# Kernel tuning notes

Hardware: AMD Instinct MI355X
Metric: run time of the kernel (lower is better)

The kernel has to match this reference:

```python
import jax, jax.numpy as jnp
import numpy as np

N = 100000   # nodes
E = 1200000  # edges
B = 128      # graphs per batch
F = 92       # raw node features
D = 64       # pre_hidden_size == gc_dim == post_hidden_size
L = 3        # n_gcn
Z = 2 * D + 1  # CGConv concat width


def setup_inputs() -> dict:
    key = jax.random.key(0)
    ks = jax.random.split(key, 24)
    s = 0.1
    inp = {
        "X": jax.random.normal(ks[0], (N, F), jnp.float32),
        "edge_idx": jax.random.randint(ks[1], (2, E), 0, N),
        "edge_weight": jax.random.uniform(ks[2], (E,), jnp.float32),
        "edge_attr": jax.random.normal(ks[3], (E,), jnp.float32),
        "batch_map": jnp.sort(jax.random.randint(ks[4], (N,), 0, B)),
        # pre-GCN MLP: F->D, D->D, D->D, relu after each
        "pre_W0": jax.random.normal(ks[5], (F, D)) * s,
        "pre_b0": jnp.zeros((D,), jnp.float32),
        "pre_W1": jax.random.normal(ks[6], (D, D)) * s,
        "pre_b1": jnp.zeros((D,), jnp.float32),
        "pre_W2": jax.random.normal(ks[7], (D, D)) * s,
        "pre_b2": jnp.zeros((D,), jnp.float32),
        # CGConv gates: lin_f / lin_s: (2D+1)->D, stacked over L layers
        "cg_Wf": jax.random.normal(ks[8], (L, Z, D)) * s,
        "cg_bf": jnp.zeros((L, D), jnp.float32),
        "cg_Ws": jax.random.normal(ks[9], (L, Z, D)) * s,
        "cg_bs": jnp.zeros((L, D), jnp.float32),
        # post-GCN MLP: D->D x3 (relu) then D->1
        "post_W0": jax.random.normal(ks[10], (D, D)) * s,
        "post_b0": jnp.zeros((D,), jnp.float32),
        "post_W1": jax.random.normal(ks[11], (D, D)) * s,
        "post_b1": jnp.zeros((D,), jnp.float32),
        "post_W2": jax.random.normal(ks[12], (D, D)) * s,
        "post_b2": jnp.zeros((D,), jnp.float32),
        "post_Wf": jax.random.normal(ks[13], (D, 1)) * s,
        "post_bf": jnp.zeros((1,), jnp.float32),
    }
    return inp


def _forward(X, edge_idx, edge_weight, edge_attr, batch_map,
             pre_W0, pre_b0, pre_W1, pre_b1, pre_W2, pre_b2,
             cg_Wf, cg_bf, cg_Ws, cg_bs,
             post_W0, post_b0, post_W1, post_b1, post_W2, post_b2,
             post_Wf, post_bf):
    relu = jax.nn.relu
    # pre-GC MLP
    h = relu(X @ pre_W0 + pre_b0)
    h = relu(h @ pre_W1 + pre_b1)
    h = relu(h @ pre_W2 + pre_b2)  # [N, D]

    src = edge_idx[0]  # x_j (message source)
    dst = edge_idx[1]  # x_i (aggregation target)
    ea = edge_attr.reshape(-1, 1)  # [E, 1]
    # in-degree for mean aggregation (nodes with no edges -> 0 via denom clamp)
    deg = jax.ops.segment_sum(jnp.ones((E,), h.dtype), dst, num_segments=N)
    denom = jnp.maximum(deg, 1.0)[:, None]  # [N, 1]

    for l in range(L):
        # CGConv: z = [x_i || x_j || e], out = x + mean_i(sigmoid(z Wf) * softplus(z Ws))
        z = jnp.concatenate([h[dst], h[src], ea], axis=-1)  # [E, 2D+1]
        m = jax.nn.sigmoid(z @ cg_Wf[l] + cg_bf[l]) * jax.nn.softplus(z @ cg_Ws[l] + cg_bs[l])
        agg = jax.ops.segment_sum(m, dst, num_segments=N) / denom
        h = relu(h + agg)  # residual + activation from pyg Sequential

    # early global mean pool per graph
    gsum = jax.ops.segment_sum(h, batch_map, num_segments=B)
    gcnt = jax.ops.segment_sum(jnp.ones((N,), h.dtype), batch_map, num_segments=B)
    g = gsum / jnp.maximum(gcnt, 1.0)[:, None]  # [B, D]

    # post-GC MLP
    g = relu(g @ post_W0 + post_b0)
    g = relu(g @ post_W1 + post_b1)
    g = relu(g @ post_W2 + post_b2)
    return g @ post_Wf + post_bf  # [B, 1]


def reference(X, edge_idx, edge_weight, edge_attr, batch_map,
              pre_W0, pre_b0, pre_W1, pre_b1, pre_W2, pre_b2,
              cg_Wf, cg_bf, cg_Ws, cg_bs,
              post_W0, post_b0, post_W1, post_b1, post_W2, post_b2,
              post_Wf, post_bf):
    return _forward(X, edge_idx, edge_weight, edge_attr, batch_map,
                    pre_W0, pre_b0, pre_W1, pre_b1, pre_W2, pre_b2,
                    cg_Wf, cg_bf, cg_Ws, cg_bs,
                    post_W0, post_b0, post_W1, post_b1, post_W2, post_b2,
                    post_Wf, post_bf)
```

## Files before the change

kernel.cpp:

```cpp
#include <hip/hip_runtime.h>
#include <hip/hip_bf16.h>
#include <math.h>

#define GN 100000
#define GE 1200000
#define GB 128
#define GF 92
#define GD 64
#define GL 3
#define GZ 129

#define HS 65

__device__ __forceinline__ unsigned int f2bf_rne(float x)
{
    unsigned int u = __float_as_uint(x);
    u += 0x7fffu + ((u >> 16) & 1u);
    return u >> 16;
}

__global__ __launch_bounds__(256, 2) void premlp_kernel(
    const float* __restrict__ X,
    const float* __restrict__ W0, const float* __restrict__ b0,
    const float* __restrict__ W1, const float* __restrict__ b1,
    const float* __restrict__ W2, const float* __restrict__ b2,
    const float* __restrict__ WfD, const float* __restrict__ WsD,
    const float* __restrict__ WfS, const float* __restrict__ WsS,
    const float* __restrict__ bf, const float* __restrict__ bs,
    float* __restrict__ hout, unsigned int* __restrict__ Pout,
    float* __restrict__ Qout, int N)
{
    __shared__ __align__(16) float Wl[5888];
    __shared__ float hl[128 * HS];
    const int tid = threadIdx.x;
    const int lane = tid & 63;
    const int col0 = (tid >> 6) * 16;
    const int base = blockIdx.x * 128;
    const int n0 = base + lane;
    const int n1 = base + 64 + lane;
    const int nn0 = (n0 < N) ? n0 : (N - 1);
    const int nn1 = (n1 < N) ? n1 : (N - 1);
    const bool act0 = (n0 < N), act1 = (n1 < N);

    float a0[16], a1[16], s0[16], s1[16];

    {
        const float4* __restrict__ s4 = (const float4*)W0;
        float4* __restrict__ d4 = (float4*)Wl;
        for (int i = tid; i < 1472; i += 256) d4[i] = s4[i];
    }
    __syncthreads();

#pragma unroll
    for (int j = 0; j < 16; ++j) { a0[j] = b0[col0 + j]; a1[j] = a0[j]; }
    {
        const float4* __restrict__ r40 = (const float4*)(X + (size_t)nn0 * GF);
        const float4* __restrict__ r41 = (const float4*)(X + (size_t)nn1 * GF);
        for (int c = 0; c < 23; ++c) {
            float4 v0 = r40[c];
            float4 v1 = r41[c];
            const float* __restrict__ w = Wl + c * 256 + col0;
#pragma unroll
            for (int j = 0; j < 16; ++j) {
                float wa = w[j], wb = w[64 + j], wc = w[128 + j], wd = w[192 + j];
                a0[j] = fmaf(v0.x, wa, a0[j]);
                a0[j] = fmaf(v0.y, wb, a0[j]);
                a0[j] = fmaf(v0.z, wc, a0[j]);
                a0[j] = fmaf(v0.w, wd, a0[j]);
                a1[j] = fmaf(v1.x, wa, a1[j]);
                a1[j] = fmaf(v1.y, wb, a1[j]);
                a1[j] = fmaf(v1.z, wc, a1[j]);
                a1[j] = fmaf(v1.w, wd, a1[j]);
            }
        }
    }
    __syncthreads();
#pragma unroll
    for (int j = 0; j < 16; ++j) {
        hl[lane * HS + col0 + j] = fmaxf(a0[j], 0.f);
        hl[(64 + lane) * HS + col0 + j] = fmaxf(a1[j], 0.f);
    }
    {
        const float4* __restrict__ s4 = (const float4*)W1;
        float4* __restrict__ d4 = (float4*)Wl;
        for (int i = tid; i < 1024; i += 256) d4[i] = s4[i];
    }
    __syncthreads();

#pragma unroll
    for (int j = 0; j < 16; ++j) { a0[j] = b1[col0 + j]; a1[j] = a0[j]; }
    for (int c = 0; c < 16; ++c) {
        float h0 = hl[lane * HS + 4 * c + 0];
        float h1 = hl[lane * HS + 4 * c + 1];
        float h2 = hl[lane * HS + 4 * c + 2];
        float h3 = hl[lane * HS + 4 * c + 3];
        float g0 = hl[(64 + lane) * HS + 4 * c + 0];
        float g1 = hl[(64 + lane) * HS + 4 * c + 1];
        float g2 = hl[(64 + lane) * HS + 4 * c + 2];
        float g3 = hl[(64 + lane) * HS + 4 * c + 3];
        const float* __restrict__ w = Wl + c * 256 + col0;
#pragma unroll
        for (int j = 0; j < 16; ++j) {
            float wa = w[j], wb = w[64 + j], wc = w[128 + j], wd = w[192 + j];
            a0[j] = fmaf(h0, wa, a0[j]);
            a0[j] = fmaf(h1, wb, a0[j]);
            a0[j] = fmaf(h2, wc, a0[j]);
            a0[j] = fmaf(h3, wd, a0[j]);
            a1[j] = fmaf(g0, wa, a1[j]);
            a1[j] = fmaf(g1, wb, a1[j]);
            a1[j] = fmaf(g2, wc, a1[j]);
            a1[j] = fmaf(g3, wd, a1[j]);
        }
    }
    __syncthreads();
#pragma unroll
    for (int j = 0; j < 16; ++j) {
        hl[lane * HS + col0 + j] = fmaxf(a0[j], 0.f);
        hl[(64 + lane) * HS + col0 + j] = fmaxf(a1[j], 0.f);
    }
    {
        const float4* __restrict__ s4 = (const float4*)W2;
        float4* __restrict__ d4 = (float4*)Wl;
        for (int i = tid; i < 1024; i += 256) d4[i] = s4[i];
    }
    __syncthreads();

#pragma unroll
    for (int j = 0; j < 16; ++j) { a0[j] = b2[col0 + j]; a1[j] = a0[j]; }
    for (int c = 0; c < 16; ++c) {
        float h0 = hl[lane * HS + 4 * c + 0];
        float h1 = hl[lane * HS + 4 * c + 1];
        float h2 = hl[lane * HS + 4 * c + 2];
        float h3 = hl[lane * HS + 4 * c + 3];
        float g0 = hl[(64 + lane) * HS + 4 * c + 0];
        float g1 = hl[(64 + lane) * HS + 4 * c + 1];
        float g2 = hl[(64 + lane) * HS + 4 * c + 2];
        float g3 = hl[(64 + lane) * HS + 4 * c + 3];
        const float* __restrict__ w = Wl + c * 256 + col0;
#pragma unroll
        for (int j = 0; j < 16; ++j) {
            float wa = w[j], wb = w[64 + j], wc = w[128 + j], wd = w[192 + j];
            a0[j] = fmaf(h0, wa, a0[j]);
            a0[j] = fmaf(h1, wb, a0[j]);
            a0[j] = fmaf(h2, wc, a0[j]);
            a0[j] = fmaf(h3, wd, a0[j]);
            a1[j] = fmaf(g0, wa, a1[j]);
            a1[j] = fmaf(g1, wb, a1[j]);
            a1[j] = fmaf(g2, wc, a1[j]);
            a1[j] = fmaf(g3, wd, a1[j]);
        }
    }
    __syncthreads();
#pragma unroll
    for (int j = 0; j < 16; ++j) {
        hl[lane * HS + col0 + j] = fmaxf(a0[j], 0.f);
        hl[(64 + lane) * HS + col0 + j] = fmaxf(a1[j], 0.f);
    }
    if (act0) {
        float4* __restrict__ op = (float4*)(hout + (size_t)n0 * 64 + col0);
#pragma unroll
        for (int q = 0; q < 4; ++q)
            op[q] = make_float4(fmaxf(a0[q * 4], 0.f), fmaxf(a0[q * 4 + 1], 0.f),
                                fmaxf(a0[q * 4 + 2], 0.f), fmaxf(a0[q * 4 + 3], 0.f));
    }
    if (act1) {
        float4* __restrict__ op = (float4*)(hout + (size_t)n1 * 64 + col0);
#pragma unroll
        for (int q = 0; q < 4; ++q)
            op[q] = make_float4(fmaxf(a1[q * 4], 0.f), fmaxf(a1[q * 4 + 1], 0.f),
                                fmaxf(a1[q * 4 + 2], 0.f), fmaxf(a1[q * 4 + 3], 0.f));
    }
    {
        const float4* __restrict__ s4 = (const float4*)WfS;
        float4* __restrict__ d4 = (float4*)Wl;
        for (int i = tid; i < 1024; i += 256) d4[i] = s4[i];
    }
    __syncthreads();

#pragma unroll
    for (int j = 0; j < 16; ++j) { a0[j] = 0.f; a1[j] = 0.f; }
    for (int c = 0; c < 16; ++c) {
        float h0 = hl[lane * HS + 4 * c + 0];
        float h1 = hl[lane * HS + 4 * c + 1];
        float h2 = hl[lane * HS + 4 * c + 2];
        float h3 = hl[lane * HS + 4 * c + 3];
        float g0 = hl[(64 + lane) * HS + 4 * c + 0];
        float g1 = hl[(64 + lane) * HS + 4 * c + 1];
        float g2 = hl[(64 + lane) * HS + 4 * c + 2];
        float g3 = hl[(64 + lane) * HS + 4 * c + 3];
        const float* __restrict__ w = Wl + c * 256 + col0;
#pragma unroll
        for (int j = 0; j < 16; ++j) {
            float wa = w[j], wb = w[64 + j], wc = w[128 + j], wd = w[192 + j];
            a0[j] = fmaf(h0, wa, a0[j]);
            a0[j] = fmaf(h1, wb, a0[j]);
            a0[j] = fmaf(h2, wc, a0[j]);
            a0[j] = fmaf(h3, wd, a0[j]);
            a1[j] = fmaf(g0, wa, a1[j]);
            a1[j] = fmaf(g1, wb, a1[j]);
            a1[j] = fmaf(g2, wc, a1[j]);
            a1[j] = fmaf(g3, wd, a1[j]);
        }
    }
    __syncthreads();
    {
        const float4* __restrict__ s4 = (const float4*)WsS;
        float4* __restrict__ d4 = (float4*)Wl;
        for (int i = tid; i < 1024; i += 256) d4[i] = s4[i];
    }
    __syncthreads();

#pragma unroll
    for (int j = 0; j < 16; ++j) { s0[j] = 0.f; s1[j] = 0.f; }
    for (int c = 0; c < 16; ++c) {
        float h0 = hl[lane * HS + 4 * c + 0];
        float h1 = hl[lane * HS + 4 * c + 1];
        float h2 = hl[lane * HS + 4 * c + 2];
        float h3 = hl[lane * HS + 4 * c + 3];
        float g0 = hl[(64 + lane) * HS + 4 * c + 0];
        float g1 = hl[(64 + lane) * HS + 4 * c + 1];
        float g2 = hl[(64 + lane) * HS + 4 * c + 2];
        float g3 = hl[(64 + lane) * HS + 4 * c + 3];
        const float* __restrict__ w = Wl + c * 256 + col0;
#pragma unroll
        for (int j = 0; j < 16; ++j) {
            float wa = w[j], wb = w[64 + j], wc = w[128 + j], wd = w[192 + j];
            s0[j] = fmaf(h0, wa, s0[j]);
            s0[j] = fmaf(h1, wb, s0[j]);
            s0[j] = fmaf(h2, wc, s0[j]);
            s0[j] = fmaf(h3, wd, s0[j]);
            s1[j] = fmaf(g0, wa, s1[j]);
            s1[j] = fmaf(g1, wb, s1[j]);
            s1[j] = fmaf(g2, wc, s1[j]);
            s1[j] = fmaf(g3, wd, s1[j]);
        }
    }
    if (act0) {
        uint4* __restrict__ pp = (uint4*)(Pout + (size_t)n0 * 64 + col0);
#pragma unroll
        for (int q = 0; q < 4; ++q) {
            uint4 pk;
            pk.x = f2bf_rne(a0[q * 4])     | (f2bf_rne(s0[q * 4]) << 16);
            pk.y = f2bf_rne(a0[q * 4 + 1]) | (f2bf_rne(s0[q * 4 + 1]) << 16);
            pk.z = f2bf_rne(a0[q * 4 + 2]) | (f2bf_rne(s0[q * 4 + 2]) << 16);
            pk.w = f2bf_rne(a0[q * 4 + 3]) | (f2bf_rne(s0[q * 4 + 3]) << 16);
            pp[q] = pk;
        }
    }
    if (act1) {
        uint4* __restrict__ pp = (uint4*)(Pout + (size_t)n1 * 64 + col0);
#pragma unroll
        for (int q = 0; q < 4; ++q) {
            uint4 pk;
            pk.x = f2bf_rne(a1[q * 4])     | (f2bf_rne(s1[q * 4]) << 16);
            pk.y = f2bf_rne(a1[q * 4 + 1]) | (f2bf_rne(s1[q * 4 + 1]) << 16);
            pk.z = f2bf_rne(a1[q * 4 + 2]) | (f2bf_rne(s1[q * 4 + 2]) << 16);
            pk.w = f2bf_rne(a1[q * 4 + 3]) | (f2bf_rne(s1[q * 4 + 3]) << 16);
            pp[q] = pk;
        }
    }
    __syncthreads();
    {
        const float4* __restrict__ s4 = (const float4*)WfD;
        float4* __restrict__ d4 = (float4*)Wl;
        for (int i = tid; i < 1024; i += 256) d4[i] = s4[i];
    }
    __syncthreads();

#pragma unroll
    for (int j = 0; j < 16; ++j) { a0[j] = bf[col0 + j]; a1[j] = a0[j]; }
    for (int c = 0; c < 16; ++c) {
        float h0 = hl[lane * HS + 4 * c + 0];
        float h1 = hl[lane * HS + 4 * c + 1];
        float h2 = hl[lane * HS + 4 * c + 2];
        float h3 = hl[lane * HS + 4 * c + 3];
        float g0 = hl[(64 + lane) * HS + 4 * c + 0];
        float g1 = hl[(64 + lane) * HS + 4 * c + 1];
        float g2 = hl[(64 + lane) * HS + 4 * c + 2];
        float g3 = hl[(64 + lane) * HS + 4 * c + 3];
        const float* __restrict__ w = Wl + c * 256 + col0;
#pragma unroll
        for (int j = 0; j < 16; ++j) {
            float wa = w[j], wb = w[64 + j], wc = w[128 + j], wd = w[192 + j];
            a0[j] = fmaf(h0, wa, a0[j]);
            a0[j] = fmaf(h1, wb, a0[j]);
            a0[j] = fmaf(h2, wc, a0[j]);
            a0[j] = fmaf(h3, wd, a0[j]);
            a1[j] = fmaf(g0, wa, a1[j]);
            a1[j] = fmaf(g1, wb, a1[j]);
            a1[j] = fmaf(g2, wc, a1[j]);
            a1[j] = fmaf(g3, wd, a1[j]);
        }
    }
    __syncthreads();
    {
        const float4* __restrict__ s4 = (const float4*)WsD;
        float4* __restrict__ d4 = (float4*)Wl;
        for (int i = tid; i < 1024; i += 256) d4[i] = s4[i];
    }
    __syncthreads();

#pragma unroll
    for (int j = 0; j < 16; ++j) { s0[j] = bs[col0 + j]; s1[j] = s0[j]; }
    for (int c = 0; c < 16; ++c) {
        float h0 = hl[lane * HS + 4 * c + 0];
        float h1 = hl[lane * HS + 4 * c + 1];
        float h2 = hl[lane * HS + 4 * c + 2];
        float h3 = hl[lane * HS + 4 * c + 3];
        float g0 = hl[(64 + lane) * HS + 4 * c + 0];
        float g1 = hl[(64 + lane) * HS + 4 * c + 1];
        float g2 = hl[(64 + lane) * HS + 4 * c + 2];
        float g3 = hl[(64 + lane) * HS + 4 * c + 3];
        const float* __restrict__ w = Wl + c * 256 + col0;
#pragma unroll
        for (int j = 0; j < 16; ++j) {
            float wa = w[j], wb = w[64 + j], wc = w[128 + j], wd = w[192 + j];
            s0[j] = fmaf(h0, wa, s0[j]);
            s0[j] = fmaf(h1, wb, s0[j]);
            s0[j] = fmaf(h2, wc, s0[j]);
            s0[j] = fmaf(h3, wd, s0[j]);
            s1[j] = fmaf(g0, wa, s1[j]);
            s1[j] = fmaf(g1, wb, s1[j]);
            s1[j] = fmaf(g2, wc, s1[j]);
            s1[j] = fmaf(g3, wd, s1[j]);
        }
    }
    if (act0) {
        float4* __restrict__ qp = (float4*)(Qout + (size_t)n0 * 128 + col0 * 2);
#pragma unroll
        for (int q = 0; q < 8; ++q)
            qp[q] = make_float4(a0[q * 2], s0[q * 2], a0[q * 2 + 1], s0[q * 2 + 1]);
    }
    if (act1) {
        float4* __restrict__ qp = (float4*)(Qout + (size_t)n1 * 128 + col0 * 2);
#pragma unroll
        for (int q = 0; q < 8; ++q)
            qp[q] = make_float4(a1[q * 2], s1[q * 2], a1[q * 2 + 1], s1[q * 2 + 1]);
    }
}

__global__ __launch_bounds__(256, 3) void pjq_kernel(
    const float* __restrict__ h,
    const float* __restrict__ Wf, const float* __restrict__ Ws,
    const float* __restrict__ bfv, const float* __restrict__ bsv,
    unsigned int* __restrict__ P, float* __restrict__ Q, int N)
{
    __shared__ __align__(16) float Wl[4096];
    __shared__ float hl[128 * HS];
    const int tid = threadIdx.x;
    const int lane = tid & 63;
    const int col0 = (tid >> 6) * 16;
    const int base = blockIdx.x * 128;
    const int n0 = base + lane;
    const int n1 = base + 64 + lane;
    const bool act0 = (n0 < N), act1 = (n1 < N);

    float a0[16], a1[16], s0[16], s1[16];

    for (int q = tid; q < 2048; q += 256) {
        int r = q >> 4, c4 = q & 15;
        int rr = base + r; rr = (rr < N) ? rr : (N - 1);
        float4 v = ((const float4*)(h + (size_t)rr * 64))[c4];
        float* dp = hl + r * HS + c4 * 4;
        dp[0] = v.x; dp[1] = v.y; dp[2] = v.z; dp[3] = v.w;
    }
    {
        const float4* __restrict__ s4 = (const float4*)(Wf + 64 * 64);
        float4* __restrict__ d4 = (float4*)Wl;
        for (int i = tid; i < 1024; i += 256) d4[i] = s4[i];
    }
    __syncthreads();

#pragma unroll
    for (int j = 0; j < 16; ++j) { a0[j] = 0.f; a1[j] = 0.f; }
    for (int c = 0; c < 16; ++c) {
        float h0 = hl[lane * HS + 4 * c + 0];
        float h1 = hl[lane * HS + 4 * c + 1];
        float h2 = hl[lane * HS + 4 * c + 2];
        float h3 = hl[lane * HS + 4 * c + 3];
        float g0 = hl[(64 + lane) * HS + 4 * c + 0];
        float g1 = hl[(64 + lane) * HS + 4 * c + 1];
        float g2 = hl[(64 + lane) * HS + 4 * c + 2];
        float g3 = hl[(64 + lane) * HS + 4 * c + 3];
        const float* __restrict__ w = Wl + c * 256 + col0;
#pragma unroll
        for (int j = 0; j < 16; ++j) {
            float wa = w[j], wb = w[64 + j], wc = w[128 + j], wd = w[192 + j];
            a0[j] = fmaf(h0, wa, a0[j]);
            a0[j] = fmaf(h1, wb, a0[j]);
            a0[j] = fmaf(h2, wc, a0[j]);
            a0[j] = fmaf(h3, wd, a0[j]);
            a1[j] = fmaf(g0, wa, a1[j]);
            a1[j] = fmaf(g1, wb, a1[j]);
            a1[j] = fmaf(g2, wc, a1[j]);
            a1[j] = fmaf(g3, wd, a1[j]);
        }
    }
    __syncthreads();
    {
        const float4* __restrict__ s4 = (const float4*)(Ws + 64 * 64);
        float4* __restrict__ d4 = (float4*)Wl;
        for (int i = tid; i < 1024; i += 256) d4[i] = s4[i];
    }
    __syncthreads();

#pragma unroll
    for (int j = 0; j < 16; ++j) { s0[j] = 0.f; s1[j] = 0.f; }
    for (int c = 0; c < 16; ++c) {
        float h0 = hl[lane * HS + 4 * c + 0];
        float h1 = hl[lane * HS + 4 * c + 1];
        float h2 = hl[lane * HS + 4 * c + 2];
        float h3 = hl[lane * HS + 4 * c + 3];
        float g0 = hl[(64 + lane) * HS + 4 * c + 0];
        float g1 = hl[(64 + lane) * HS + 4 * c + 1];
        float g2 = hl[(64 + lane) * HS + 4 * c + 2];
        float g3 = hl[(64 + lane) * HS + 4 * c + 3];
        const float* __restrict__ w = Wl + c * 256 + col0;
#pragma unroll
        for (int j = 0; j < 16; ++j) {
            float wa = w[j], wb = w[64 + j], wc = w[128 + j], wd = w[192 + j];
            s0[j] = fmaf(h0, wa, s0[j]);
            s0[j] = fmaf(h1, wb, s0[j]);
            s0[j] = fmaf(h2, wc, s0[j]);
            s0[j] = fmaf(h3, wd, s0[j]);
            s1[j] = fmaf(g0, wa, s1[j]);
            s1[j] = fmaf(g1, wb, s1[j]);
            s1[j] = fmaf(g2, wc, s1[j]);
            s1[j] = fmaf(g3, wd, s1[j]);
        }
    }
    if (act0) {
        uint4* __restrict__ pp = (uint4*)(P + (size_t)n0 * 64 + col0);
#pragma unroll
        for (int q = 0; q < 4; ++q) {
            uint4 pk;
            pk.x = f2bf_rne(a0[q * 4])     | (f2bf_rne(s0[q * 4]) << 16);
            pk.y = f2bf_rne(a0[q * 4 + 1]) | (f2bf_rne(s0[q * 4 + 1]) << 16);
            pk.z = f2bf_rne(a0[q * 4 + 2]) | (f2bf_rne(s0[q * 4 + 2]) << 16);
            pk.w = f2bf_rne(a0[q * 4 + 3]) | (f2bf_rne(s0[q * 4 + 3]) << 16);
            pp[q] = pk;
        }
    }
    if (act1) {
        uint4* __restrict__ pp = (uint4*)(P + (size_t)n1 * 64 + col0);
#pragma unroll
        for (int q = 0; q < 4; ++q) {
            uint4 pk;
            pk.x = f2bf_rne(a1[q * 4])     | (f2bf_rne(s1[q * 4]) << 16);
            pk.y = f2bf_rne(a1[q * 4 + 1]) | (f2bf_rne(s1[q * 4 + 1]) << 16);
            pk.z = f2bf_rne(a1[q * 4 + 2]) | (f2bf_rne(s1[q * 4 + 2]) << 16);
            pk.w = f2bf_rne(a1[q * 4 + 3]) | (f2bf_rne(s1[q * 4 + 3]) << 16);
            pp[q] = pk;
        }
    }
    __syncthreads();
    {
        const float4* __restrict__ s4 = (const float4*)Wf;
        float4* __restrict__ d4 = (float4*)Wl;
        for (int i = tid; i < 1024; i += 256) d4[i] = s4[i];
    }
    __syncthreads();

#pragma unroll
    for (int j = 0; j < 16; ++j) { a0[j] = bfv[col0 + j]; a1[j] = a0[j]; }
    for (int c = 0; c < 16; ++c) {
        float h0 = hl[lane * HS + 4 * c + 0];
        float h1 = hl[lane * HS + 4 * c + 1];
        float h2 = hl[lane * HS + 4 * c + 2];
        float h3 = hl[lane * HS + 4 * c + 3];
        float g0 = hl[(64 + lane) * HS + 4 * c + 0];
        float g1 = hl[(64 + lane) * HS + 4 * c + 1];
        float g2 = hl[(64 + lane) * HS + 4 * c + 2];
        float g3 = hl[(64 + lane) * HS + 4 * c + 3];
        const float* __restrict__ w = Wl + c * 256 + col0;
#pragma unroll
        for (int j = 0; j < 16; ++j) {
            float wa = w[j], wb = w[64 + j], wc = w[128 + j], wd = w[192 + j];
            a0[j] = fmaf(h0, wa, a0[j]);
            a0[j] = fmaf(h1, wb, a0[j]);
            a0[j] = fmaf(h2, wc, a0[j]);
            a0[j] = fmaf(h3, wd, a0[j]);
            a1[j] = fmaf(g0, wa, a1[j]);
            a1[j] = fmaf(g1, wb, a1[j]);
            a1[j] = fmaf(g2, wc, a1[j]);
            a1[j] = fmaf(g3, wd, a1[j]);
        }
    }
    __syncthreads();
    {
        const float4* __restrict__ s4 = (const float4*)Ws;
        float4* __restrict__ d4 = (float4*)Wl;
        for (int i = tid; i < 1024; i += 256) d4[i] = s4[i];
    }
    __syncthreads();

#pragma unroll
    for (int j = 0; j < 16; ++j) { s0[j] = bsv[col0 + j]; s1[j] = s0[j]; }
    for (int c = 0; c < 16; ++c) {
        float h0 = hl[lane * HS + 4 * c + 0];
        float h1 = hl[lane * HS + 4 * c + 1];
        float h2 = hl[lane * HS + 4 * c + 2];
        float h3 = hl[lane * HS + 4 * c + 3];
        float g0 = hl[(64 + lane) * HS + 4 * c + 0];
        float g1 = hl[(64 + lane) * HS + 4 * c + 1];
        float g2 = hl[(64 + lane) * HS + 4 * c + 2];
        float g3 = hl[(64 + lane) * HS + 4 * c + 3];
        const float* __restrict__ w = Wl + c * 256 + col0;
#pragma unroll
        for (int j = 0; j < 16; ++j) {
            float wa = w[j], wb = w[64 + j], wc = w[128 + j], wd = w[192 + j];
            s0[j] = fmaf(h0, wa, s0[j]);
            s0[j] = fmaf(h1, wb, s0[j]);
            s0[j] = fmaf(h2, wc, s0[j]);
            s0[j] = fmaf(h3, wd, s0[j]);
            s1[j] = fmaf(g0, wa, s1[j]);
            s1[j] = fmaf(g1, wb, s1[j]);
            s1[j] = fmaf(g2, wc, s1[j]);
            s1[j] = fmaf(g3, wd, s1[j]);
        }
    }
    if (act0) {
        float4* __restrict__ qp = (float4*)(Q + (size_t)n0 * 128 + col0 * 2);
#pragma unroll
        for (int q = 0; q < 8; ++q)
            qp[q] = make_float4(a0[q * 2], s0[q * 2], a0[q * 2 + 1], s0[q * 2 + 1]);
    }
    if (act1) {
        float4* __restrict__ qp = (float4*)(Q + (size_t)n1 * 128 + col0 * 2);
#pragma unroll
        for (int q = 0; q < 8; ++q)
            qp[q] = make_float4(a1[q * 2], s1[q * 2], a1[q * 2 + 1], s1[q * 2 + 1]);
    }
}

__global__ __launch_bounds__(256) void deg_kernel(
    const int* __restrict__ dst, int* __restrict__ deg, int E)
{
    int e = blockIdx.x * blockDim.x + threadIdx.x;
    if (e < E) atomicAdd(&deg[dst[e]], 1);
}

__global__ __launch_bounds__(1024) void scanA_kernel(
    const int* __restrict__ deg, int* __restrict__ iscan,
    int* __restrict__ bsum, int N)
{
    __shared__ int lds[1024];
    int tid = threadIdx.x;
    int gid = blockIdx.x * 1024 + tid;
    int v = (gid < N) ? deg[gid] : 0;
    lds[tid] = v; __syncthreads();
    for (int off = 1; off < 1024; off <<= 1) {
        int t = (tid >= off) ? lds[tid - off] : 0;
        __syncthreads();
        lds[tid] += t;
        __syncthreads();
    }
    if (gid < N) iscan[gid] = lds[tid];
    if (tid == 1023) bsum[blockIdx.x] = lds[1023];
}

__global__ __launch_bounds__(128) void scanB_kernel(
    const int* __restrict__ bsum, int* __restrict__ boff, int nb)
{
    __shared__ int lds[128];
    int t = threadIdx.x;
    int v = (t < nb) ? bsum[t] : 0;
    lds[t] = v; __syncthreads();
    for (int off = 1; off < 128; off <<= 1) {
        int u = (t >= off) ? lds[t - off] : 0;
        __syncthreads();
        lds[t] += u;
        __syncthreads();
    }
    if (t < nb) boff[t] = lds[t] - v;
}

__global__ __launch_bounds__(256) void scanC_kernel(
    const int* __restrict__ iscan, const int* __restrict__ boff,
    const int* __restrict__ deg,
    int* __restrict__ rowptr, int* __restrict__ cursor, int N)
{
    int i = blockIdx.x * blockDim.x + threadIdx.x;
    if (i >= N) return;
    int incl = iscan[i] + boff[i >> 10];
    rowptr[i + 1] = incl;
    cursor[i] = incl - deg[i];
    if (i == 0) rowptr[0] = 0;
}

__global__ __launch_bounds__(256) void escatter_kernel(
    const int* __restrict__ src, const int* __restrict__ dst,
    const float* __restrict__ ea, int* __restrict__ cursor,
    int2* __restrict__ e_se, int E)
{
    int e = blockIdx.x * blockDim.x + threadIdx.x;
    if (e >= E) return;
    int pos = atomicAdd(&cursor[dst[e]], 1);
    e_se[pos] = make_int2(src[e], __float_as_int(ea[e]));
}

__global__ __launch_bounds__(256) void edge_kernel(
    const float* __restrict__ h, const int* __restrict__ rowptr,
    const int2* __restrict__ e_se,
    const unsigned int* __restrict__ P,
    const float* __restrict__ Q,
    const float* __restrict__ Wf, const float* __restrict__ Ws,
    float* __restrict__ hout)
{
    int n = blockIdx.x * 4 + (threadIdx.x >> 6);
    int d = threadIdx.x & 63;

    const float2 qv = ((const float2*)Q)[(size_t)n * 64 + d];
    float qf = qv.x, qs = qv.y;
    float wf = Wf[128 * 64 + d];
    float ws = Ws[128 * 64 + d];

    size_t idx = (size_t)n * 64 + d;
    float hres = h[idx];

    int rb = rowptr[n], re = rowptr[n + 1];
    float agg = 0.f;
#pragma unroll 8
    for (int p = rb; p < re; ++p) {
        int2 se = e_se[p];
        int s = se.x;
        float ea = __int_as_float(se.y);
        unsigned int pv = P[(size_t)s * 64 + d];
        float pf = __uint_as_float(pv << 16);
        float psv = __uint_as_float(pv & 0xffff0000u);
        float xF = fmaf(ea, wf, qf + pf);
        float xS = fmaf(ea, ws, qs + psv);
        float sig = __builtin_amdgcn_rcpf(1.f + __expf(-xF));
        float t = __expf(-fabsf(xS));
        float sp = fmaxf(xS, 0.f) + __logf(1.f + t);
        agg = fmaf(sig, sp, agg);
    }

    float inv = 1.f / (float)max(re - rb, 1);
    hout[idx] = fmaxf(hres + agg * inv, 0.f);
}

__global__ __launch_bounds__(256) void gstart_kernel(
    const int* __restrict__ bm, int* __restrict__ gstart, int N)
{
    int i = blockIdx.x * blockDim.x + threadIdx.x;
    if (i >= N) return;
    int b = bm[i];
    int prev = (i == 0) ? -1 : bm[i - 1];
    for (int g = prev + 1; g <= b; ++g) gstart[g] = i;
    if (i == N - 1)
        for (int g = b + 1; g <= GB; ++g) gstart[g] = N;
}

__global__ __launch_bounds__(256) void pool_seg_kernel(
    const float* __restrict__ h, const int* __restrict__ gstart,
    float* __restrict__ g)
{
    int b = blockIdx.x;
    int s = gstart[b], e = gstart[b + 1];
    int d = threadIdx.x & 63;
    int w = threadIdx.x >> 6;
    float acc = 0.f;
    for (int n = s + w; n < e; n += 4)
        acc += h[(size_t)n * 64 + d];
    __shared__ float lds[256];
    lds[threadIdx.x] = acc;
    __syncthreads();
    if (w == 0) {
        acc = lds[d] + lds[64 + d] + lds[128 + d] + lds[192 + d];
        g[b * 64 + d] = acc / fmaxf((float)(e - s), 1.f);
    }
}

__global__ __launch_bounds__(256) void postmlp_kernel(
    const float* __restrict__ g,
    const float* __restrict__ W0, const float* __restrict__ b0,
    const float* __restrict__ W1, const float* __restrict__ b1,
    const float* __restrict__ W2, const float* __restrict__ b2,
    const float* __restrict__ Wfin, const float* __restrict__ bfin,
    float* __restrict__ out)
{
    int b = blockIdx.x * 4 + (threadIdx.x >> 6);
    int d = threadIdx.x & 63;
    float h = g[(size_t)b * 64 + d];

    float acc = b0[d];
#pragma unroll
    for (int k = 0; k < 64; ++k)
        acc = fmaf(__shfl(h, k, 64), W0[k * 64 + d], acc);
    h = fmaxf(acc, 0.f);

    acc = b1[d];
#pragma unroll
    for (int k = 0; k < 64; ++k)
        acc = fmaf(__shfl(h, k, 64), W1[k * 64 + d], acc);
    h = fmaxf(acc, 0.f);

    acc = b2[d];
#pragma unroll
    for (int k = 0; k < 64; ++k)
        acc = fmaf(__shfl(h, k, 64), W2[k * 64 + d], acc);
    h = fmaxf(acc, 0.f);

    float v = h * Wfin[d];
#pragma unroll
    for (int off = 32; off >= 1; off >>= 1)
        v += __shfl_xor(v, off, 64);
    if (d == 0) out[b] = v + bfin[0];
}

extern "C" void kernel_launch(void* const* d_in, const int* in_sizes, int n_in,
                              void* d_out, int out_size, void* d_ws, size_t ws_size,
                              hipStream_t stream)
{
    const float* X      = (const float*)d_in[0];
    const int*   eidx   = (const int*)d_in[1];
    const float* ea     = (const float*)d_in[3];
    const int*   bm     = (const int*)d_in[4];
    const float* pre_W0 = (const float*)d_in[5];
    const float* pre_b0 = (const float*)d_in[6];
    const float* pre_W1 = (const float*)d_in[7];
    const float* pre_b1 = (const float*)d_in[8];
    const float* pre_W2 = (const float*)d_in[9];
    const float* pre_b2 = (const float*)d_in[10];
    const float* cg_Wf  = (const float*)d_in[11];
    const float* cg_bf  = (const float*)d_in[12];
    const float* cg_Ws  = (const float*)d_in[13];
    const float* cg_bs  = (const float*)d_in[14];
    const float* post_W0 = (const float*)d_in[15];
    const float* post_b0 = (const float*)d_in[16];
    const float* post_W1 = (const float*)d_in[17];
    const float* post_b1 = (const float*)d_in[18];
    const float* post_W2 = (const float*)d_in[19];
    const float* post_b2 = (const float*)d_in[20];
    const float* post_Wf = (const float*)d_in[21];
    const float* post_bf = (const float*)d_in[22];

    const int* src = eidx;
    const int* dst = eidx + GE;

    const size_t N64 = (size_t)GN * 64;
    float* hA    = (float*)d_ws;
    float* hB    = hA + N64;
    unsigned int* P = (unsigned int*)(hB + N64);
    int* deg_i   = (int*)(P + N64);
    int* iscan   = deg_i + GN;
    int* bsum    = iscan + GN;
    int* boff    = bsum + 128;
    int* rowptr  = boff + 128;
    int* cursor  = rowptr + GN + 2;
    int2* e_se   = (int2*)(cursor + GN);
    int* gstart  = (int*)(e_se + GE);
    float* g0    = (float*)(gstart + GB + 1);
    float* Q     = g0 + (size_t)GB * 64;

    const int TPB = 256;
    int gridE  = (GE + TPB - 1) / TPB;
    int gridN  = (GN + TPB - 1) / TPB;
    int gridP  = (GN + 127) / 128;
    int gridND = ((GN * 64) + TPB - 1) / TPB;
    int scanBlocks = (GN + 1023) / 1024;

    const float* Wf0 = cg_Wf;
    const float* Ws0 = cg_Ws;
    const float* Wf1 = cg_Wf + (size_t)1 * GZ * GD;
    const float* Ws1 = cg_Ws + (size_t)1 * GZ * GD;
    const float* Wf2 = cg_Wf + (size_t)2 * GZ * GD;
    const float* Ws2 = cg_Ws + (size_t)2 * GZ * GD;

    premlp_kernel<<<gridP, TPB, 0, stream>>>(
        X, pre_W0, pre_b0, pre_W1, pre_b1, pre_W2, pre_b2,
        Wf0, Ws0, Wf0 + 64 * 64, Ws0 + 64 * 64, cg_bf, cg_bs,
        hA, P, Q, GN);

    hipMemsetAsync(deg_i, 0, GN * sizeof(int), stream);
    deg_kernel<<<gridE, TPB, 0, stream>>>(dst, deg_i, GE);
    scanA_kernel<<<scanBlocks, 1024, 0, stream>>>(deg_i, iscan, bsum, GN);
    scanB_kernel<<<1, 128, 0, stream>>>(bsum, boff, scanBlocks);
    scanC_kernel<<<gridN, TPB, 0, stream>>>(iscan, boff, deg_i, rowptr, cursor, GN);
    escatter_kernel<<<gridE, TPB, 0, stream>>>(src, dst, ea, cursor, e_se, GE);

    gstart_kernel<<<gridN, TPB, 0, stream>>>(bm, gstart, GN);

    edge_kernel<<<gridND, TPB, 0, stream>>>(
        hA, rowptr, e_se, P, Q, Wf0, Ws0, hB);
    pjq_kernel<<<gridP, TPB, 0, stream>>>(
        hB, Wf1, Ws1, cg_bf + GD, cg_bs + GD, P, Q, GN);
    edge_kernel<<<gridND, TPB, 0, stream>>>(
        hB, rowptr, e_se, P, Q, Wf1, Ws1, hA);
    pjq_kernel<<<gridP, TPB, 0, stream>>>(
        hA, Wf2, Ws2, cg_bf + 2 * GD, cg_bs + 2 * GD, P, Q, GN);
    edge_kernel<<<gridND, TPB, 0, stream>>>(
        hA, rowptr, e_se, P, Q, Wf2, Ws2, hB);

    pool_seg_kernel<<<GB, TPB, 0, stream>>>(hB, gstart, g0);

    postmlp_kernel<<<GB / 4, TPB, 0, stream>>>(
        g0, post_W0, post_b0, post_W1, post_b1, post_W2, post_b2,
        post_Wf, post_bf, (float*)d_out);
}
```

Baseline: 884.0 us.

## Switch CGConv aggregation to edge-parallel chunks with atomic segment flushes

Replaces the node-per-wavefront edge loop with an edge-parallel kernel. Each wavefront processes a fixed chunk of 32 dst-sorted edges and flushes partial sums via atomicAdd when the destination changes. A separate finalize kernel applies the mean, residual and ReLU, then re-zeroes the accumulator. This targets load imbalance from the variable in-degree, at the cost of float atomics, a wider 16-byte edge record, an extra N×64 buffer and one extra kernel launch per layer.

```diff
diff --git a/kernel.cpp b/kernel.cpp
--- a/kernel.cpp
+++ b/kernel.cpp
@@ -11,6 +11,7 @@
 #define GZ 129
 
 #define HS 65
+#define EC 32
 
 __device__ __forceinline__ unsigned int f2bf_rne(float x)
 {
@@ -591,41 +592,44 @@
 __global__ __launch_bounds__(256) void escatter_kernel(
     const int* __restrict__ src, const int* __restrict__ dst,
     const float* __restrict__ ea, int* __restrict__ cursor,
-    int2* __restrict__ e_se, int E)
+    int4* __restrict__ e_sd, int E)
 {
     int e = blockIdx.x * blockDim.x + threadIdx.x;
     if (e >= E) return;
-    int pos = atomicAdd(&cursor[dst[e]], 1);
-    e_se[pos] = make_int2(src[e], __float_as_int(ea[e]));
-}
-
-__global__ __launch_bounds__(256) void edge_kernel(
-    const float* __restrict__ h, const int* __restrict__ rowptr,
-    const int2* __restrict__ e_se,
+    int d = dst[e];
+    int pos = atomicAdd(&cursor[d], 1);
+    e_sd[pos] = make_int4(src[e], __float_as_int(ea[e]), d, 0);
+}
+
+__global__ __launch_bounds__(256) void edgepar_kernel(
+    const int4* __restrict__ e_sd,
     const unsigned int* __restrict__ P,
     const float* __restrict__ Q,
     const float* __restrict__ Wf, const float* __restrict__ Ws,
-    float* __restrict__ hout)
-{
-    int n = blockIdx.x * 4 + (threadIdx.x >> 6);
-    int d = threadIdx.x & 63;
-
-    const float2 qv = ((const float2*)Q)[(size_t)n * 64 + d];
-    float qf = qv.x, qs = qv.y;
-    float wf = Wf[128 * 64 + d];
-    float ws = Ws[128 * 64 + d];
-
-    size_t idx = (size_t)n * 64 + d;
-    float hres = h[idx];
-
-    int rb = rowptr[n], re = rowptr[n + 1];
-    float agg = 0.f;
-#pragma unroll 8
-    for (int p = rb; p < re; ++p) {
-        int2 se = e_se[p];
-        int s = se.x;
+    float* __restrict__ agg, int E)
+{
+    const int lane = threadIdx.x & 63;
+    const int wid = blockIdx.x * 4 + (threadIdx.x >> 6);
+    int c0 = wid * EC;
+    if (c0 >= E) return;
+    int ce = min(c0 + EC, E);
+
+    const float wf = Wf[128 * 64 + lane];
+    const float ws = Ws[128 * 64 + lane];
+
+    int cur = -1;
+    float acc = 0.f, qf = 0.f, qs = 0.f;
+    for (int c = c0; c < ce; ++c) {
+        int4 se = e_sd[c];
+        unsigned int pv = P[(size_t)se.x * 64 + lane];
+        if (se.z != cur) {
+            if (cur >= 0) atomicAdd(&agg[(size_t)cur * 64 + lane], acc);
+            acc = 0.f;
+            cur = se.z;
+            float2 qv = ((const float2*)Q)[(size_t)cur * 64 + lane];
+            qf = qv.x; qs = qv.y;
+        }
         float ea = __int_as_float(se.y);
-        unsigned int pv = P[(size_t)s * 64 + d];
         float pf = __uint_as_float(pv << 16);
         float psv = __uint_as_float(pv & 0xffff0000u);
         float xF = fmaf(ea, wf, qf + pf);
@@ -633,11 +637,22 @@
         float sig = __builtin_amdgcn_rcpf(1.f + __expf(-xF));
         float t = __expf(-fabsf(xS));
         float sp = fmaxf(xS, 0.f) + __logf(1.f + t);
-        agg = fmaf(sig, sp, agg);
-    }
-
-    float inv = 1.f / (float)max(re - rb, 1);
-    hout[idx] = fmaxf(hres + agg * inv, 0.f);
+        acc = fmaf(sig, sp, acc);
+    }
+    atomicAdd(&agg[(size_t)cur * 64 + lane], acc);
+}
+
+__global__ __launch_bounds__(256) void finalize_kernel(
+    const float* __restrict__ hin, const int* __restrict__ deg,
+    float* __restrict__ agg, float* __restrict__ hout, int total)
+{
+    int i = blockIdx.x * 256 + threadIdx.x;
+    if (i >= total) return;
+    int n = i >> 6;
+    float a = agg[i];
+    agg[i] = 0.f;
+    float inv = 1.f / (float)max(deg[n], 1);
+    hout[i] = fmaxf(hin[i] + a * inv, 0.f);
 }
 
 __global__ __launch_bounds__(256) void gstart_kernel(
@@ -743,22 +758,24 @@
     float* hA    = (float*)d_ws;
     float* hB    = hA + N64;
     unsigned int* P = (unsigned int*)(hB + N64);
-    int* deg_i   = (int*)(P + N64);
+    float* agg   = (float*)(P + N64);
+    float* Q     = agg + N64;
+    int4* e_sd   = (int4*)(Q + (size_t)GN * 128);
+    int* deg_i   = (int*)(e_sd + GE);
     int* iscan   = deg_i + GN;
     int* bsum    = iscan + GN;
     int* boff    = bsum + 128;
     int* rowptr  = boff + 128;
     int* cursor  = rowptr + GN + 2;
-    int2* e_se   = (int2*)(cursor + GN);
-    int* gstart  = (int*)(e_se + GE);
+    int* gstart  = cursor + GN;
     float* g0    = (float*)(gstart + GB + 1);
-    float* Q     = g0 + (size_t)GB * 64;
 
     const int TPB = 256;
     int gridE  = (GE + TPB - 1) / TPB;
     int gridN  = (GN + TPB - 1) / TPB;
     int gridP  = (GN + 127) / 128;
     int gridND = ((GN * 64) + TPB - 1) / TPB;
+    int gridEP = (GE + EC * 4 - 1) / (EC * 4);
     int scanBlocks = (GN + 1023) / 1024;
 
     const float* Wf0 = cg_Wf;
@@ -774,24 +791,27 @@
         hA, P, Q, GN);
 
     hipMemsetAsync(deg_i, 0, GN * sizeof(int), stream);
+    hipMemsetAsync(agg, 0, N64 * sizeof(float), stream);
     deg_kernel<<<gridE, TPB, 0, stream>>>(dst, deg_i, GE);
     scanA_kernel<<<scanBlocks, 1024, 0, stream>>>(deg_i, iscan, bsum, GN);
     scanB_kernel<<<1, 128, 0, stream>>>(bsum, boff, scanBlocks);
     scanC_kernel<<<gridN, TPB, 0, stream>>>(iscan, boff, deg_i, rowptr, cursor, GN);
-    escatter_kernel<<<gridE, TPB, 0, stream>>>(src, dst, ea, cursor, e_se, GE);
+    escatter_kernel<<<gridE, TPB, 0, stream>>>(src, dst, ea, cursor, e_sd, GE);
 
     gstart_kernel<<<gridN, TPB, 0, stream>>>(bm, gstart, GN);
 
-    edge_kernel<<<gridND, TPB, 0, stream>>>(
-        hA, rowptr, e_se, P, Q, Wf0, Ws0, hB);
+    edgepar_kernel<<<gridEP, TPB, 0, stream>>>(e_sd, P, Q, Wf0, Ws0, agg, GE);
+    finalize_kernel<<<gridND, TPB, 0, stream>>>(hA, deg_i, agg, hB, GN * 64);
     pjq_kernel<<<gridP, TPB, 0, stream>>>(
         hB, Wf1, Ws1, cg_bf + GD, cg_bs + GD, P, Q, GN);
-    edge_kernel<<<gridND, TPB, 0, stream>>>(
-        hB, rowptr, e_se, P, Q, Wf1, Ws1, hA);
+
+    edgepar_kernel<<<gridEP, TPB, 0, stream>>>(e_sd, P, Q, Wf1, Ws1, agg, GE);
+    finalize_kernel<<<gridND, TPB, 0, stream>>>(hB, deg_i, agg, hA, GN * 64);
     pjq_kernel<<<gridP, TPB, 0, stream>>>(
         hA, Wf2, Ws2, cg_bf + 2 * GD, cg_bs + 2 * GD, P, Q, GN);
-    edge_kernel<<<gridND, TPB, 0, stream>>>(
-        hA, rowptr, e_se, P, Q, Wf2, Ws2, hB);
+
+    edgepar_kernel<<<gridEP, TPB, 0, stream>>>(e_sd, P, Q, Wf2, Ws2, agg, GE);
+    finalize_kernel<<<gridND, TPB, 0, stream>>>(hA, deg_i, agg, hB, GN * 64);
 
     pool_seg_kernel<<<GB, TPB, 0, stream>>>(hB, gstart, g0);
 
```

After: 1.038 ms. +17.4%, slower.

## Fuse f/s gate GEMMs in pjq kernel and read h rows directly from global

Applied to the files above, without the earlier changes.

The pjq kernel now stages the Wf and Ws tiles together in a doubled shared buffer and computes both gate projections in one pass, instead of four sequential weight loads separated by barriers. It also drops the shared-memory staging of h: each thread reads its node's row straight from global memory as float4, so all four wavefronts in a block reload the same rows. This removes several barriers and the h LDS traffic. In exchange, register pressure rises (64 live accumulators under launch_bounds 256,3) and global h reads are repeated across wavefronts and across the two passes.

```diff
diff --git a/kernel.cpp b/kernel.cpp
--- a/kernel.cpp
+++ b/kernel.cpp
@@ -345,88 +345,60 @@
     const float* __restrict__ bfv, const float* __restrict__ bsv,
     unsigned int* __restrict__ P, float* __restrict__ Q, int N)
 {
-    __shared__ __align__(16) float Wl[4096];
-    __shared__ float hl[128 * HS];
+    __shared__ __align__(16) float Wl[8192];
     const int tid = threadIdx.x;
     const int lane = tid & 63;
     const int col0 = (tid >> 6) * 16;
     const int base = blockIdx.x * 128;
     const int n0 = base + lane;
     const int n1 = base + 64 + lane;
+    const int nn0 = (n0 < N) ? n0 : (N - 1);
+    const int nn1 = (n1 < N) ? n1 : (N - 1);
     const bool act0 = (n0 < N), act1 = (n1 < N);
 
-    float a0[16], a1[16], s0[16], s1[16];
-
-    for (int q = tid; q < 2048; q += 256) {
-        int r = q >> 4, c4 = q & 15;
-        int rr = base + r; rr = (rr < N) ? rr : (N - 1);
-        float4 v = ((const float4*)(h + (size_t)rr * 64))[c4];
-        float* dp = hl + r * HS + c4 * 4;
-        dp[0] = v.x; dp[1] = v.y; dp[2] = v.z; dp[3] = v.w;
-    }
-    {
-        const float4* __restrict__ s4 = (const float4*)(Wf + 64 * 64);
-        float4* __restrict__ d4 = (float4*)Wl;
-        for (int i = tid; i < 1024; i += 256) d4[i] = s4[i];
-    }
-    __syncthreads();
-
-#pragma unroll
-    for (int j = 0; j < 16; ++j) { a0[j] = 0.f; a1[j] = 0.f; }
+    const float4* __restrict__ h40 = (const float4*)(h + (size_t)nn0 * 64);
+    const float4* __restrict__ h41 = (const float4*)(h + (size_t)nn1 * 64);
+
+    float aF0[16], aF1[16], aS0[16], aS1[16];
+
+    {
+        const float4* __restrict__ f4 = (const float4*)(Wf + 64 * 64);
+        const float4* __restrict__ s4 = (const float4*)(Ws + 64 * 64);
+        float4* __restrict__ d4 = (float4*)Wl;
+        for (int i = tid; i < 1024; i += 256) {
+            d4[i] = f4[i];
+            d4[1024 + i] = s4[i];
+        }
+    }
+    __syncthreads();
+
+#pragma unroll
+    for (int j = 0; j < 16; ++j) { aF0[j] = 0.f; aF1[j] = 0.f; aS0[j] = 0.f; aS1[j] = 0.f; }
     for (int c = 0; c < 16; ++c) {
-        float h0 = hl[lane * HS + 4 * c + 0];
-        float h1 = hl[lane * HS + 4 * c + 1];
-        float h2 = hl[lane * HS + 4 * c + 2];
-        float h3 = hl[lane * HS + 4 * c + 3];
-        float g0 = hl[(64 + lane) * HS + 4 * c + 0];
-        float g1 = hl[(64 + lane) * HS + 4 * c + 1];
-        float g2 = hl[(64 + lane) * HS + 4 * c + 2];
-        float g3 = hl[(64 + lane) * HS + 4 * c + 3];
-        const float* __restrict__ w = Wl + c * 256 + col0;
+        float4 v0 = h40[c];
+        float4 v1 = h41[c];
+        const float* __restrict__ wf = Wl + c * 256 + col0;
+        const float* __restrict__ ws = Wl + 4096 + c * 256 + col0;
 #pragma unroll
         for (int j = 0; j < 16; ++j) {
-            float wa = w[j], wb = w[64 + j], wc = w[128 + j], wd = w[192 + j];
-            a0[j] = fmaf(h0, wa, a0[j]);
-            a0[j] = fmaf(h1, wb, a0[j]);
-            a0[j] = fmaf(h2, wc, a0[j]);
-            a0[j] = fmaf(h3, wd, a0[j]);
-            a1[j] = fmaf(g0, wa, a1[j]);
-            a1[j] = fmaf(g1, wb, a1[j]);
-            a1[j] = fmaf(g2, wc, a1[j]);
-            a1[j] = fmaf(g3, wd, a1[j]);
-        }
-    }
-    __syncthreads();
-    {
-        const float4* __restrict__ s4 = (const float4*)(Ws + 64 * 64);
-        float4* __restrict__ d4 = (float4*)Wl;
-        for (int i = tid; i < 1024; i += 256) d4[i] = s4[i];
-    }
-    __syncthreads();
-
-#pragma unroll
-    for (int j = 0; j < 16; ++j) { s0[j] = 0.f; s1[j] = 0.f; }
-    for (int c = 0; c < 16; ++c) {
-        float h0 = hl[lane * HS + 4 * c + 0];
-        float h1 = hl[lane * HS + 4 * c + 1];
-        float h2 = hl[lane * HS + 4 * c + 2];
-        float h3 = hl[lane * HS + 4 * c + 3];
-        float g0 = hl[(64 + lane) * HS + 4 * c + 0];
-        float g1 = hl[(64 + lane) * HS + 4 * c + 1];
-        float g2 = hl[(64 + lane) * HS + 4 * c + 2];
-        float g3 = hl[(64 + lane) * HS + 4 * c + 3];
-        const float* __restrict__ w = Wl + c * 256 + col0;
-#pragma unroll
-        for (int j = 0; j < 16; ++j) {
-            float wa = w[j], wb = w[64 + j], wc = w[128 + j], wd = w[192 + j];
-            s0[j] = fmaf(h0, wa, s0[j]);
-            s0[j] = fmaf(h1, wb, s0[j]);
-            s0[j] = fmaf(h2, wc, s0[j]);
-            s0[j] = fmaf(h3, wd, s0[j]);
-            s1[j] = fmaf(g0, wa, s1[j]);
-            s1[j] = fmaf(g1, wb, s1[j]);
-            s1[j] = fmaf(g2, wc, s1[j]);
-            s1[j] = fmaf(g3, wd, s1[j]);
+            float wa = wf[j], wb = wf[64 + j], wc = wf[128 + j], wd = wf[192 + j];
+            aF0[j] = fmaf(v0.x, wa, aF0[j]);
+            aF0[j] = fmaf(v0.y, wb, aF0[j]);
+            aF0[j] = fmaf(v0.z, wc, aF0[j]);
+            aF0[j] = fmaf(v0.w, wd, aF0[j]);
+            aF1[j] = fmaf(v1.x, wa, aF1[j]);
+            aF1[j] = fmaf(v1.y, wb, aF1[j]);
+            aF1[j] = fmaf(v1.z, wc, aF1[j]);
+            aF1[j] = fmaf(v1.w, wd, aF1[j]);
+            float sa = ws[j], sb = ws[64 + j], sc = ws[128 + j], sd = ws[192 + j];
+            aS0[j] = fmaf(v0.x, sa, aS0[j]);
+            aS0[j] = fmaf(v0.y, sb, aS0[j]);
+            aS0[j] = fmaf(v0.z, sc, aS0[j]);
+            aS0[j] = fmaf(v0.w, sd, aS0[j]);
+            aS1[j] = fmaf(v1.x, sa, aS1[j]);
+            aS1[j] = fmaf(v1.y, sb, aS1[j]);
+            aS1[j] = fmaf(v1.z, sc, aS1[j]);
+            aS1[j] = fmaf(v1.w, sd, aS1[j]);
         }
     }
     if (act0) {
@@ -434,10 +406,10 @@
 #pragma unroll
         for (int q = 0; q < 4; ++q) {
             uint4 pk;
-            pk.x = f2bf_rne(a0[q * 4])     | (f2bf_rne(s0[q * 4]) << 16);
-            pk.y = f2bf_rne(a0[q * 4 + 1]) | (f2bf_rne(s0[q * 4 + 1]) << 16);
-            pk.z = f2bf_rne(a0[q * 4 + 2]) | (f2bf_rne(s0[q * 4 + 2]) << 16);
-            pk.w = f2bf_rne(a0[q * 4 + 3]) | (f2bf_rne(s0[q * 4 + 3]) << 16);
+            pk.x = f2bf_rne(aF0[q * 4])     | (f2bf_rne(aS0[q * 4]) << 16);
+            pk.y = f2bf_rne(aF0[q * 4 + 1]) | (f2bf_rne(aS0[q * 4 + 1]) << 16);
+            pk.z = f2bf_rne(aF0[q * 4 + 2]) | (f2bf_rne(aS0[q * 4 + 2]) << 16);
+            pk.w = f2bf_rne(aF0[q * 4 + 3]) | (f2bf_rne(aS0[q * 4 + 3]) << 16);
             pp[q] = pk;
         }
     }
@@ -446,90 +418,69 @@
 #pragma unroll
         for (int q = 0; q < 4; ++q) {
             uint4 pk;
-            pk.x = f2bf_rne(a1[q * 4])     | (f2bf_rne(s1[q * 4]) << 16);
-            pk.y = f2bf_rne(a1[q * 4 + 1]) | (f2bf_rne(s1[q * 4 + 1]) << 16);
-            pk.z = f2bf_rne(a1[q * 4 + 2]) | (f2bf_rne(s1[q * 4 + 2]) << 16);
-            pk.w = f2bf_rne(a1[q * 4 + 3]) | (f2bf_rne(s1[q * 4 + 3]) << 16);
+            pk.x = f2bf_rne(aF1[q * 4])     | (f2bf_rne(aS1[q * 4]) << 16);
+            pk.y = f2bf_rne(aF1[q * 4 + 1]) | (f2bf_rne(aS1[q * 4 + 1]) << 16);
+            pk.z = f2bf_rne(aF1[q * 4 + 2]) | (f2bf_rne(aS1[q * 4 + 2]) << 16);
+            pk.w = f2bf_rne(aF1[q * 4 + 3]) | (f2bf_rne(aS1[q * 4 + 3]) << 16);
             pp[q] = pk;
         }
     }
     __syncthreads();
-    {
-        const float4* __restrict__ s4 = (const float4*)Wf;
-        float4* __restrict__ d4 = (float4*)Wl;
-        for (int i = tid; i < 1024; i += 256) d4[i] = s4[i];
-    }
-    __syncthreads();
-
-#pragma unroll
-    for (int j = 0; j < 16; ++j) { a0[j] = bfv[col0 + j]; a1[j] = a0[j]; }
+
+    {
+        const float4* __restrict__ f4 = (const float4*)Wf;
+        const float4* __restrict__ s4 = (const float4*)Ws;
+        float4* __restrict__ d4 = (float4*)Wl;
+        for (int i = tid; i < 1024; i += 256) {
+            d4[i] = f4[i];
+            d4[1024 + i] = s4[i];
+        }
+    }
+    __syncthreads();
+
+#pragma unroll
+    for (int j = 0; j < 16; ++j) {
+        aF0[j] = bfv[col0 + j]; aF1[j] = aF0[j];
+        aS0[j] = bsv[col0 + j]; aS1[j] = aS0[j];
+    }
     for (int c = 0; c < 16; ++c) {
-        float h0 = hl[lane * HS + 4 * c + 0];
-        float h1 = hl[lane * HS + 4 * c + 1];
-        float h2 = hl[lane * HS + 4 * c + 2];
-        float h3 = hl[lane * HS + 4 * c + 3];
-        float g0 = hl[(64 + lane) * HS + 4 * c + 0];
-        float g1 = hl[(64 + lane) * HS + 4 * c + 1];
-        float g2 = hl[(64 + lane) * HS + 4 * c + 2];
-        float g3 = hl[(64 + lane) * HS + 4 * c + 3];
-        const float* __restrict__ w = Wl + c * 256 + col0;
+        float4 v0 = h40[c];
+        float4 v1 = h41[c];
+        const float* __restrict__ wf = Wl + c * 256 + col0;
+        const float* __restrict__ ws = Wl + 4096 + c * 256 + col0;
 #pragma unroll
         for (int j = 0; j < 16; ++j) {
-            float wa = w[j], wb = w[64 + j], wc = w[128 + j], wd = w[192 + j];
-            a0[j] = fmaf(h0, wa, a0[j]);
-            a0[j] = fmaf(h1, wb, a0[j]);
-            a0[j] = fmaf(h2, wc, a0[j]);
-            a0[j] = fmaf(h3, wd, a0[j]);
-            a1[j] = fmaf(g0, wa, a1[j]);
-            a1[j] = fmaf(g1, wb, a1[j]);
-            a1[j] = fmaf(g2, wc, a1[j]);
-            a1[j] = fmaf(g3, wd, a1[j]);
-        }
-    }
-    __syncthreads();
-    {
-        const float4* __restrict__ s4 = (const float4*)Ws;
-        float4* __restrict__ d4 = (float4*)Wl;
-        for (int i = tid; i < 1024; i += 256) d4[i] = s4[i];
-    }
-    __syncthreads();
-
-#pragma unroll
-    for (int j = 0; j < 16; ++j) { s0[j] = bsv[col0 + j]; s1[j] = s0[j]; }
-    for (int c = 0; c < 16; ++c) {
-        float h0 = hl[lane * HS + 4 * c + 0];
-        float h1 = hl[lane * HS + 4 * c + 1];
-        float h2 = hl[lane * HS + 4 * c + 2];
-        float h3 = hl[lane * HS + 4 * c + 3];
-        float g0 = hl[(64 + lane) * HS + 4 * c + 0];
-        float g1 = hl[(64 + lane) * HS + 4 * c + 1];
-        float g2 = hl[(64 + lane) * HS + 4 * c + 2];
-        float g3 = hl[(64 + lane) * HS + 4 * c + 3];
-        const float* __restrict__ w = Wl + c * 256 + col0;
-#pragma unroll
-        for (int j = 0; j < 16; ++j) {
-            float wa = w[j], wb = w[64 + j], wc = w[128 + j], wd = w[192 + j];
-            s0[j] = fmaf(h0, wa, s0[j]);
-            s0[j] = fmaf(h1, wb, s0[j]);
-            s0[j] = fmaf(h2, wc, s0[j]);
-            s0[j] = fmaf(h3, wd, s0[j]);
-            s1[j] = fmaf(g0, wa, s1[j]);
-            s1[j] = fmaf(g1, wb, s1[j]);
-            s1[j] = fmaf(g2, wc, s1[j]);
-            s1[j] = fmaf(g3, wd, s1[j]);
+            float wa = wf[j], wb = wf[64 + j], wc = wf[128 + j], wd = wf[192 + j];
+            aF0[j] = fmaf(v0.x, wa, aF0[j]);
+            aF0[j] = fmaf(v0.y, wb, aF0[j]);
+            aF0[j] = fmaf(v0.z, wc, aF0[j]);
+            aF0[j] = fmaf(v0.w, wd, aF0[j]);
+            aF1[j] = fmaf(v1.x, wa, aF1[j]);
+            aF1[j] = fmaf(v1.y, wb, aF1[j]);
+            aF1[j] = fmaf(v1.z, wc, aF1[j]);
+            aF1[j] = fmaf(v1.w, wd, aF1[j]);
+            float sa = ws[j], sb = ws[64 + j], sc = ws[128 + j], sd = ws[192 + j];
+            aS0[j] = fmaf(v0.x, sa, aS0[j]);
+            aS0[j] = fmaf(v0.y, sb, aS0[j]);
+            aS0[j] = fmaf(v0.z, sc, aS0[j]);
+            aS0[j] = fmaf(v0.w, sd, aS0[j]);
+            aS1[j] = fmaf(v1.x, sa, aS1[j]);
+            aS1[j] = fmaf(v1.y, sb, aS1[j]);
+            aS1[j] = fmaf(v1.z, sc, aS1[j]);
+            aS1[j] = fmaf(v1.w, sd, aS1[j]);
         }
     }
     if (act0) {
         float4* __restrict__ qp = (float4*)(Q + (size_t)n0 * 128 + col0 * 2);
 #pragma unroll
         for (int q = 0; q < 8; ++q)
-            qp[q] = make_float4(a0[q * 2], s0[q * 2], a0[q * 2 + 1], s0[q * 2 + 1]);
+            qp[q] = make_float4(aF0[q * 2], aS0[q * 2], aF0[q * 2 + 1], aS0[q * 2 + 1]);
     }
     if (act1) {
         float4* __restrict__ qp = (float4*)(Q + (size_t)n1 * 128 + col0 * 2);
 #pragma unroll
         for (int q = 0; q < 8; ++q)
-            qp[q] = make_float4(a1[q * 2], s1[q * 2], a1[q * 2 + 1], s1[q * 2 + 1]);
+            qp[q] = make_float4(aF1[q * 2], aS1[q * 2], aF1[q * 2 + 1], aS1[q * 2 + 1]);
     }
 }
 
```

Result: no change. 889.1 us (+0.6%).
